# Performance work log

Hardware: AMD Instinct MI355X
Metric: run time of the kernel (lower is better)

## Reference

```python
import jax, jax.numpy as jnp
import numpy as np

NUM_HEADS = 16
HEAD_DIM = 64


def setup_inputs() -> dict:
    key = jax.random.key(0)
    ks = jax.random.split(key, 6)
    B, S, E = 4, 1024, 1024
    return {
        "x": jax.random.normal(ks[0], (B, S, E), dtype=jnp.float32),
        "W_qkv": jax.random.normal(ks[1], (E, 3 * E), dtype=jnp.float32) * 0.02,
        "b_qkv": jax.random.normal(ks[2], (3 * E,), dtype=jnp.float32) * 0.02,
        "pe": jax.random.normal(ks[3], (S, S, HEAD_DIM), dtype=jnp.float32) * 0.02,
        "W_out": jax.random.normal(ks[4], (E, E), dtype=jnp.float32) * 0.02,
        "b_out": jax.random.normal(ks[5], (E,), dtype=jnp.float32) * 0.02,
    }


def reference(x, W_qkv, b_qkv, pe, W_out, b_out):
    B, S, E = x.shape
    H, D = NUM_HEADS, HEAD_DIM
    scale = D ** -0.5
    # qkv projection: (B,S,3E) -> (3,B,H,S,D)
    qkv = (x @ W_qkv + b_qkv).reshape(B, S, 3, H, D).transpose(2, 0, 3, 1, 4)
    q, k, v = qkv[0], qkv[1], qkv[2]
    # raw scaled scores (NO softmax in original module)
    scores = jnp.einsum('bhxd,bhyd->bhxy', q, k) * scale
    # relative position bias: pe is (S,S,D) == (x,y,c); original permutes to (c,x,y)
    # then einsum('cxy,bnxc->bnxy', pe, q) -> equivalent to 'xyc,bhxc->bhxy'
    pe_q = jnp.einsum('xyc,bhxc->bhxy', pe, q) * scale
    attn = (scores + pe_q) @ v                      # (B,H,S,D)
    out = attn.transpose(0, 2, 1, 3).reshape(B, S, E)
    return out @ W_out + b_out
```

## Files before the change

### kernel.cpp

```cpp
#include <hip/hip_runtime.h>
#include <cstdint>
#include <cstddef>


typedef unsigned short u16;
typedef unsigned char  u8;
typedef __bf16 bf16x8 __attribute__((ext_vector_type(8)));
typedef float  f32x4  __attribute__((ext_vector_type(4)));
typedef unsigned short u16x8 __attribute__((ext_vector_type(8)));

#define MFMA16(a, b, c) __builtin_amdgcn_mfma_f32_16x16x32_bf16((a), (b), (c), 0, 0, 0)

#define GLOAD16(g, l)                                                        \
    __builtin_amdgcn_global_load_lds(                                        \
        (const __attribute__((address_space(1))) unsigned int*)(g),          \
        (__attribute__((address_space(3))) unsigned int*)(l), 16, 0, 0)

__device__ __forceinline__ u16 f2bf(float f) {
    __bf16 h = (__bf16)f;
    return __builtin_bit_cast(u16, h);
}
__device__ __forceinline__ u16x8 pack8(float4 a, float4 b) {
    u16x8 v;
    v[0] = f2bf(a.x); v[1] = f2bf(a.y); v[2] = f2bf(a.z); v[3] = f2bf(a.w);
    v[4] = f2bf(b.x); v[5] = f2bf(b.y); v[6] = f2bf(b.z); v[7] = f2bf(b.w);
    return v;
}

__device__ __forceinline__ void convT_tile(const float* __restrict__ in,
                                           u16* __restrict__ out, int R, int C,
                                           int bx, int by, float (*tile)[68]) {
    const int t  = threadIdx.x;
    const int r0 = by * 64, c0 = bx * 64;
    const int rr = t >> 4, c4 = t & 15;
    for (int p = 0; p < 4; ++p) {
        int r = rr + p * 16;
        float4 v = *(const float4*)&in[(size_t)(r0 + r) * C + c0 + c4 * 4];
        *(float4*)&tile[r][c4 * 4] = v;
    }
    __syncthreads();
    for (int p = 0; p < 4; ++p) {
        int n = rr + p * 16;
        ushort4 o;
        o.x = f2bf(tile[c4 * 4 + 0][n]);
        o.y = f2bf(tile[c4 * 4 + 1][n]);
        o.z = f2bf(tile[c4 * 4 + 2][n]);
        o.w = f2bf(tile[c4 * 4 + 3][n]);
        *(ushort4*)&out[(size_t)(c0 + n) * R + r0 + c4 * 4] = o;
    }
}

__global__ __launch_bounds__(256) void kprep(const float* __restrict__ x,
                                             u16* __restrict__ xb,
                                             const float* __restrict__ Wqkv,
                                             u16* __restrict__ wqkvT,
                                             const float* __restrict__ Wout,
                                             u16* __restrict__ woutT) {
    __shared__ float tile[64][68];
    const int bid = blockIdx.x;
    if (bid < 2048) {
        int i = (bid * 256 + threadIdx.x) * 8;
        float4 f0 = *(const float4*)&x[i];
        float4 f1 = *(const float4*)&x[i + 4];
        *(u16x8*)&xb[i] = pack8(f0, f1);
    } else if (bid < 2816) {
        int r = bid - 2048;
        convT_tile(Wqkv, wqkvT, 1024, 3072, r % 48, r / 48, tile);
    } else {
        int r = bid - 2816;
        convT_tile(Wout, woutT, 1024, 1024, r % 16, r / 16, tile);
    }
}

__global__ __launch_bounds__(256, 2) void kgemm_qkv(const u16* __restrict__ A,
                                                    const u16* __restrict__ WT,
                                                    const float* __restrict__ bias,
                                                    u16* __restrict__ qb,
                                                    u16* __restrict__ kb,
                                                    u16* __restrict__ vtb) {
    __shared__ u16 a_s[128 * 64];
    __shared__ u16 b_s[128 * 64];
    const int t = threadIdx.x;
    const int m0 = blockIdx.y * 128, n0 = blockIdx.x * 128;
    const int lane = t & 63, w = t >> 6, lm = lane & 15, lq = lane >> 4;
    const int mb = (w >> 1) * 64, nb = (w & 1) * 64;
    const int sr = t >> 3, sc = (t & 7) * 8;

    f32x4 acc[4][4] = {};
    for (int k0 = 0; k0 < 1024; k0 += 64) {
        __syncthreads();
#pragma unroll
        for (int p = 0; p < 4; ++p) {
            GLOAD16(&A [(size_t)(m0 + p * 32 + sr) * 1024 + k0 + sc], &a_s[p * 2048 + t * 8]);
            GLOAD16(&WT[(size_t)(n0 + p * 32 + sr) * 1024 + k0 + sc], &b_s[p * 2048 + t * 8]);
        }
        __syncthreads();
#pragma unroll
        for (int ks = 0; ks < 2; ++ks) {
            bf16x8 af[4], bfr[4];
#pragma unroll
            for (int mt = 0; mt < 4; ++mt)
                af[mt] = *(const bf16x8*)&a_s[(mb + mt * 16 + lm) * 64 + ks * 32 + lq * 8];
#pragma unroll
            for (int nt = 0; nt < 4; ++nt)
                bfr[nt] = *(const bf16x8*)&b_s[(nb + nt * 16 + lm) * 64 + ks * 32 + lq * 8];
#pragma unroll
            for (int mt = 0; mt < 4; ++mt)
#pragma unroll
                for (int nt = 0; nt < 4; ++nt)
                    acc[mt][nt] = MFMA16(af[mt], bfr[nt], acc[mt][nt]);
        }
    }
    for (int nt = 0; nt < 4; ++nt) {
        int col = n0 + nb + nt * 16 + lm;
        float bv = bias[col];
        int which = col >> 10;
        int h = (col >> 6) & 15, d = col & 63;
        for (int mt = 0; mt < 4; ++mt) {
            int row0 = m0 + mb + mt * 16 + lq * 4;
            int b = row0 >> 10, s = row0 & 1023;
            if (which == 2) {
                ushort4 o;
                o.x = f2bf(acc[mt][nt][0] + bv);
                o.y = f2bf(acc[mt][nt][1] + bv);
                o.z = f2bf(acc[mt][nt][2] + bv);
                o.w = f2bf(acc[mt][nt][3] + bv);
                *(ushort4*)&vtb[((size_t)(b * 16 + h) * 64 + d) * 1024 + s] = o;
            } else {
                u16* dst = (which == 0) ? qb : kb;
                for (int i = 0; i < 4; ++i)
                    dst[((size_t)((b * 16 + h) * 1024 + s + i)) * 64 + d] =
                        f2bf(acc[mt][nt][i] + bv);
            }
        }
    }
}

__global__ __launch_bounds__(256, 4) void kpq(const u16* __restrict__ qb,
                                              const float* __restrict__ pe,
                                              u8* __restrict__ Pq) {
    __shared__ u16 q_s[64 * 64];
    __shared__ u16 pe_s[2][64 * 80];
    const int x = blockIdx.x;
    const int t = threadIdx.x;
    const int lane = t & 63, w = t >> 6, lm = lane & 15, lq = lane >> 4;
#pragma unroll
    for (int p = 0; p < 2; ++p)
        GLOAD16(&qb[(size_t)((p * 32 + (t >> 3)) * 1024 + x) * 64 + (t & 7) * 8],
                &q_s[p * 2048 + t * 8]);
    const int yl = t >> 2, cq = (t & 3) * 16;
    const float* pex = pe + (size_t)x * 65536;
    float4 r0, r1, r2, r3;
    {
        const float* src = &pex[(size_t)yl * 64 + cq];
        r0 = *(const float4*)&src[0];  r1 = *(const float4*)&src[4];
        r2 = *(const float4*)&src[8];  r3 = *(const float4*)&src[12];
    }
    u8* pq_base = Pq + ((size_t)lm * 1024 + x) * 1024 + lq * 16 + w * 4;
    int cur = 0;
    for (int it = 0; it < 16; ++it) {
        *(u16x8*)&pe_s[cur][yl * 80 + cq]     = pack8(r0, r1);
        *(u16x8*)&pe_s[cur][yl * 80 + cq + 8] = pack8(r2, r3);
        __syncthreads();
        if (it < 15) {
            const float* src = &pex[(size_t)((it + 1) * 64 + yl) * 64 + cq];
            r0 = *(const float4*)&src[0];  r1 = *(const float4*)&src[4];
            r2 = *(const float4*)&src[8];  r3 = *(const float4*)&src[12];
        }
        f32x4 acc[4] = {};
#pragma unroll
        for (int ks = 0; ks < 2; ++ks) {
            bf16x8 a = *(const bf16x8*)&pe_s[cur][(16 * w + lm) * 80 + ks * 32 + lq * 8];
#pragma unroll
            for (int nt = 0; nt < 4; ++nt) {
                bf16x8 b = *(const bf16x8*)&q_s[(nt * 16 + lm) * 64 + ks * 32 + lq * 8];
                acc[nt] = MFMA16(a, b, acc[nt]);
            }
        }
#pragma unroll
        for (int nt = 0; nt < 4; ++nt) {
            unsigned int pw;
            pw = __builtin_amdgcn_cvt_pk_fp8_f32(acc[nt][0], acc[nt][1], 0u, false);
            pw = __builtin_amdgcn_cvt_pk_fp8_f32(acc[nt][2], acc[nt][3], pw, true);
            *(unsigned int*)&pq_base[(size_t)nt * 16 * 1024 * 1024 + it * 64] = pw;
        }
        cur ^= 1;
    }
}

__global__ __launch_bounds__(256, 2) void kattn(const u16* __restrict__ qb,
                                                const u16* __restrict__ kb,
                                                const u16* __restrict__ vt,
                                                const u8* __restrict__ Pq,
                                                u16* __restrict__ attnb) {
    __shared__ u16 q_s[128 * 64];
    __shared__ u16 k_s[64 * 64];
    __shared__ u16 v_s[64 * 64];
    __shared__ u16 s_s[128 * 80];
    const int bid = blockIdx.x;
    const int bh = bid & 63, x0 = (bid >> 6) * 128;
    const int t = threadIdx.x;
    const int lane = t & 63, w = t >> 6, lm = lane & 15, lq = lane >> 4;
    const int sr = t >> 3, sc = (t & 7) * 8;

#pragma unroll
    for (int p = 0; p < 4; ++p)
        GLOAD16(&qb[(size_t)(bh * 1024 + x0 + p * 32 + sr) * 64 + sc],
                &q_s[p * 2048 + t * 8]);

    const u8* PqRow = Pq + ((size_t)(bh * 1024) + x0 + 32 * w + lm) * 1024 + lq * 16;
    f32x4 oacc[2][4] = {};
    for (int y0 = 0; y0 < 1024; y0 += 64) {
        uint4 pq4[2];
#pragma unroll
        for (int nt = 0; nt < 2; ++nt)
            pq4[nt] = *(const uint4*)&PqRow[(size_t)(nt * 16) * 1024 + y0];
        __syncthreads();
#pragma unroll
        for (int p = 0; p < 2; ++p) {
            GLOAD16(&kb[(size_t)(bh * 1024 + y0 + p * 32 + sr) * 64 + sc],
                    &k_s[p * 2048 + t * 8]);
            GLOAD16(&vt[(size_t)(bh * 64 + p * 32 + sr) * 1024 + y0 + sc],
                    &v_s[p * 2048 + t * 8]);
        }
        __syncthreads();
        f32x4 sacc[4][2] = {};
#pragma unroll
        for (int ks = 0; ks < 2; ++ks) {
            bf16x8 bq[2];
#pragma unroll
            for (int nt = 0; nt < 2; ++nt)
                bq[nt] = *(const bf16x8*)&q_s[(32 * w + nt * 16 + lm) * 64 + ks * 32 + lq * 8];
#pragma unroll
            for (int mt = 0; mt < 4; ++mt) {
                bf16x8 ak = *(const bf16x8*)&k_s[(mt * 16 + lm) * 64 + ks * 32 + lq * 8];
#pragma unroll
                for (int nt = 0; nt < 2; ++nt)
                    sacc[mt][nt] = MFMA16(ak, bq[nt], sacc[mt][nt]);
            }
        }
#pragma unroll
        for (int nt = 0; nt < 2; ++nt) {
            int xl = 32 * w + nt * 16 + lm;
            const unsigned int* pqc = (const unsigned int*)&pq4[nt];
#pragma unroll
            for (int mt = 0; mt < 4; ++mt) {
                unsigned int pw = pqc[mt];
                ushort4 o;
                o.x = f2bf((sacc[mt][nt][0] + __builtin_amdgcn_cvt_f32_fp8(pw, 0)) * 0.125f);
                o.y = f2bf((sacc[mt][nt][1] + __builtin_amdgcn_cvt_f32_fp8(pw, 1)) * 0.125f);
                o.z = f2bf((sacc[mt][nt][2] + __builtin_amdgcn_cvt_f32_fp8(pw, 2)) * 0.125f);
                o.w = f2bf((sacc[mt][nt][3] + __builtin_amdgcn_cvt_f32_fp8(pw, 3)) * 0.125f);
                *(ushort4*)&s_s[xl * 80 + mt * 16 + lq * 4] = o;
            }
        }
#pragma unroll
        for (int ks = 0; ks < 2; ++ks) {
            bf16x8 as[2];
#pragma unroll
            for (int mt = 0; mt < 2; ++mt)
                as[mt] = *(const bf16x8*)&s_s[(32 * w + mt * 16 + lm) * 80 + ks * 32 + lq * 8];
#pragma unroll
            for (int nt = 0; nt < 4; ++nt) {
                bf16x8 bv = *(const bf16x8*)&v_s[(nt * 16 + lm) * 64 + ks * 32 + lq * 8];
#pragma unroll
                for (int mt = 0; mt < 2; ++mt)
                    oacc[mt][nt] = MFMA16(as[mt], bv, oacc[mt][nt]);
            }
        }
    }
    const int b = bh >> 4, h = bh & 15;
    for (int mt = 0; mt < 2; ++mt) {
        for (int nt = 0; nt < 4; ++nt) {
            int d = nt * 16 + lm;
            for (int i = 0; i < 4; ++i) {
                int s = x0 + 32 * w + mt * 16 + lq * 4 + i;
                attnb[((size_t)(b * 1024 + s)) * 1024 + h * 64 + d] = f2bf(oacc[mt][nt][i]);
            }
        }
    }
}

__global__ __launch_bounds__(256, 2) void kgemm_out(const u16* __restrict__ A,
                                                    const u16* __restrict__ WT,
                                                    const float* __restrict__ bias,
                                                    float* __restrict__ out) {
    __shared__ u16 a_s[128 * 64];
    __shared__ u16 b_s[128 * 64];
    const int t = threadIdx.x;
    const int m0 = blockIdx.y * 128, n0 = blockIdx.x * 128;
    const int lane = t & 63, w = t >> 6, lm = lane & 15, lq = lane >> 4;
    const int mb = (w >> 1) * 64, nb = (w & 1) * 64;
    const int sr = t >> 3, sc = (t & 7) * 8;

    f32x4 acc[4][4] = {};
    for (int k0 = 0; k0 < 1024; k0 += 64) {
        __syncthreads();
#pragma unroll
        for (int p = 0; p < 4; ++p) {
            GLOAD16(&A [(size_t)(m0 + p * 32 + sr) * 1024 + k0 + sc], &a_s[p * 2048 + t * 8]);
            GLOAD16(&WT[(size_t)(n0 + p * 32 + sr) * 1024 + k0 + sc], &b_s[p * 2048 + t * 8]);
        }
        __syncthreads();
#pragma unroll
        for (int ks = 0; ks < 2; ++ks) {
            bf16x8 af[4], bfr[4];
#pragma unroll
            for (int mt = 0; mt < 4; ++mt)
                af[mt] = *(const bf16x8*)&a_s[(mb + mt * 16 + lm) * 64 + ks * 32 + lq * 8];
#pragma unroll
            for (int nt = 0; nt < 4; ++nt)
                bfr[nt] = *(const bf16x8*)&b_s[(nb + nt * 16 + lm) * 64 + ks * 32 + lq * 8];
#pragma unroll
            for (int mt = 0; mt < 4; ++mt)
#pragma unroll
                for (int nt = 0; nt < 4; ++nt)
                    acc[mt][nt] = MFMA16(af[mt], bfr[nt], acc[mt][nt]);
        }
    }
    for (int nt = 0; nt < 4; ++nt) {
        int col = n0 + nb + nt * 16 + lm;
        float bv = bias[col];
        for (int mt = 0; mt < 4; ++mt) {
            for (int i = 0; i < 4; ++i) {
                int row = m0 + mb + mt * 16 + lq * 4 + i;
                out[(size_t)row * 1024 + col] = acc[mt][nt][i] + bv;
            }
        }
    }
}

extern "C" void kernel_launch(void* const* d_in, const int* in_sizes, int n_in,
                              void* d_out, int out_size, void* d_ws, size_t ws_size,
                              hipStream_t stream) {
    (void)in_sizes; (void)n_in; (void)out_size; (void)ws_size;
    const float* x    = (const float*)d_in[0];
    const float* Wqkv = (const float*)d_in[1];
    const float* bqkv = (const float*)d_in[2];
    const float* pe   = (const float*)d_in[3];
    const float* Wout = (const float*)d_in[4];
    const float* bout = (const float*)d_in[5];
    float* out = (float*)d_out;

    char* ws = (char*)d_ws;
    u16* xb    = (u16*)ws;  ws += (size_t)4096 * 1024 * 2;
    u16* wqkvT = (u16*)ws;  ws += (size_t)3072 * 1024 * 2;
    u16* woutT = (u16*)ws;  ws += (size_t)1024 * 1024 * 2;
    u16* qb    = (u16*)ws;  ws += (size_t)64 * 1024 * 64 * 2;
    u16* kb    = (u16*)ws;  ws += (size_t)64 * 1024 * 64 * 2;
    u16* vtb   = (u16*)ws;  ws += (size_t)64 * 64 * 1024 * 2;
    u16* attnb = (u16*)ws;  ws += (size_t)4 * 1024 * 1024 * 2;
    u8*  pq    = (u8*)ws;   ws += (size_t)64 * 1024 * 1024;

    kprep<<<3072, 256, 0, stream>>>(x, xb, Wqkv, wqkvT, Wout, woutT);
    kgemm_qkv<<<dim3(24, 32), 256, 0, stream>>>(xb, wqkvT, bqkv, qb, kb, vtb);
    kpq<<<1024, 256, 0, stream>>>(qb, pe, pq);
    kattn<<<512, 256, 0, stream>>>(qb, kb, vtb, pq, attnb);
    kgemm_out<<<dim3(8, 32), 256, 0, stream>>>(attnb, woutT, bout, out);
}
```

Baseline: 521.8 us.

## Rewrite QKV GEMM with 256x256 tiles and 4-stage async LDS pipeline

Restructures the QKV projection GEMM to use 512-thread blocks computing 256x256 output tiles, with a four-deep ring of LDS buffers filled by direct global-to-LDS loads issued several k-steps ahead. Raw s_barrier plus explicit vmcnt waits and s_setprio around MFMA bursts replace the per-iteration __syncthreads load/compute serialization. The aim is to hide global load latency and raise arithmetic intensity per block. The cost is only 192 blocks, which may underfill the GPU, along with higher register pressure from 32 accumulators per wave.

```diff
diff --git a/kernel.cpp b/kernel.cpp
--- a/kernel.cpp
+++ b/kernel.cpp
@@ -25,6 +25,16 @@
     v[0] = f2bf(a.x); v[1] = f2bf(a.y); v[2] = f2bf(a.z); v[3] = f2bf(a.w);
     v[4] = f2bf(b.x); v[5] = f2bf(b.y); v[6] = f2bf(b.z); v[7] = f2bf(b.w);
     return v;
+}
+
+__device__ __forceinline__ void sbar() {
+    asm volatile("" ::: "memory");
+    __builtin_amdgcn_s_barrier();
+    asm volatile("" ::: "memory");
+}
+template <int N> __device__ __forceinline__ void waitv() {
+    if constexpr (N >= 0)
+        asm volatile("s_waitcnt vmcnt(%0)" :: "n"(N) : "memory");
 }
 
 __device__ __forceinline__ void convT_tile(const float* __restrict__ in,
@@ -72,65 +82,104 @@
     }
 }
 
-__global__ __launch_bounds__(256, 2) void kgemm_qkv(const u16* __restrict__ A,
+#define STAGE_A(kt) {                                                         \
+    u16* d_ = &a_s[(kt) & 3][t * 8];                                          \
+    const u16* g_ = &A[(size_t)(m0g + (t >> 2)) * 1024 + (kt) * 32 + (t & 3) * 8]; \
+    GLOAD16(g_, d_);                                                          \
+    GLOAD16(g_ + (size_t)128 * 1024, d_ + 4096); }
+
+#define STAGE_B(kt) {                                                         \
+    u16* d_ = &b_s[(kt) & 3][t * 8];                                          \
+    const u16* g_ = &WT[(size_t)(n0g + (t >> 2)) * 1024 + (kt) * 32 + (t & 3) * 8]; \
+    GLOAD16(g_, d_);                                                          \
+    GLOAD16(g_ + (size_t)128 * 1024, d_ + 4096); }
+
+#define QKV_GROUP(g, DOSTAGE, GATEN)                                          \
+  {                                                                           \
+    const int s_ = (g) & 3;                                                   \
+                                       \
+    _Pragma("unroll")                                                         \
+    for (int mf = 0; mf < 4; ++mf)                                            \
+      af[mf] = *(const bf16x8*)&a_s[s_][(wr * 128 + mf * 16 + lm) * 32 + lq * 8]; \
+    _Pragma("unroll")                                                         \
+    for (int nf = 0; nf < 4; ++nf)                                            \
+      bfr[nf] = *(const bf16x8*)&b_s[s_][(wc * 64 + nf * 16 + lm) * 32 + lq * 8]; \
+    if (DOSTAGE) STAGE_A((g) + 3);                                            \
+    sbar();                                                                   \
+    __builtin_amdgcn_s_setprio(1);                                            \
+    _Pragma("unroll")                                                         \
+    for (int mf = 0; mf < 4; ++mf)                                            \
+      _Pragma("unroll")                                                       \
+      for (int nf = 0; nf < 4; ++nf)                                          \
+        acc[mf][nf] = MFMA16(af[mf], bfr[nf], acc[mf][nf]);                   \
+    __builtin_amdgcn_s_setprio(0);                                            \
+    sbar();                                                                   \
+                  \
+    _Pragma("unroll")                                                         \
+    for (int mf = 0; mf < 4; ++mf)                                            \
+      af[mf] = *(const bf16x8*)&a_s[s_][(wr * 128 + 64 + mf * 16 + lm) * 32 + lq * 8]; \
+    if (DOSTAGE) STAGE_B((g) + 3);                                            \
+    waitv<GATEN>();                                                           \
+    sbar();                                                                   \
+    __builtin_amdgcn_s_setprio(1);                                            \
+    _Pragma("unroll")                                                         \
+    for (int mf = 0; mf < 4; ++mf)                                            \
+      _Pragma("unroll")                                                       \
+      for (int nf = 0; nf < 4; ++nf)                                          \
+        acc[4 + mf][nf] = MFMA16(af[mf], bfr[nf], acc[4 + mf][nf]);           \
+    __builtin_amdgcn_s_setprio(0);                                            \
+    sbar();                                                                   \
+  }
+
+__global__ __launch_bounds__(512, 2) void kgemm_qkv(const u16* __restrict__ A,
                                                     const u16* __restrict__ WT,
                                                     const float* __restrict__ bias,
                                                     u16* __restrict__ qb,
                                                     u16* __restrict__ kb,
                                                     u16* __restrict__ vtb) {
-    __shared__ u16 a_s[128 * 64];
-    __shared__ u16 b_s[128 * 64];
+    __shared__ u16 a_s[4][256 * 32];
+    __shared__ u16 b_s[4][256 * 32];
     const int t = threadIdx.x;
-    const int m0 = blockIdx.y * 128, n0 = blockIdx.x * 128;
+    const int m0g = blockIdx.y * 256, n0g = blockIdx.x * 256;
     const int lane = t & 63, w = t >> 6, lm = lane & 15, lq = lane >> 4;
-    const int mb = (w >> 1) * 64, nb = (w & 1) * 64;
-    const int sr = t >> 3, sc = (t & 7) * 8;
-
-    f32x4 acc[4][4] = {};
-    for (int k0 = 0; k0 < 1024; k0 += 64) {
-        __syncthreads();
-#pragma unroll
-        for (int p = 0; p < 4; ++p) {
-            GLOAD16(&A [(size_t)(m0 + p * 32 + sr) * 1024 + k0 + sc], &a_s[p * 2048 + t * 8]);
-            GLOAD16(&WT[(size_t)(n0 + p * 32 + sr) * 1024 + k0 + sc], &b_s[p * 2048 + t * 8]);
-        }
-        __syncthreads();
-#pragma unroll
-        for (int ks = 0; ks < 2; ++ks) {
-            bf16x8 af[4], bfr[4];
-#pragma unroll
-            for (int mt = 0; mt < 4; ++mt)
-                af[mt] = *(const bf16x8*)&a_s[(mb + mt * 16 + lm) * 64 + ks * 32 + lq * 8];
-#pragma unroll
-            for (int nt = 0; nt < 4; ++nt)
-                bfr[nt] = *(const bf16x8*)&b_s[(nb + nt * 16 + lm) * 64 + ks * 32 + lq * 8];
-#pragma unroll
-            for (int mt = 0; mt < 4; ++mt)
-#pragma unroll
-                for (int nt = 0; nt < 4; ++nt)
-                    acc[mt][nt] = MFMA16(af[mt], bfr[nt], acc[mt][nt]);
-        }
-    }
-    for (int nt = 0; nt < 4; ++nt) {
-        int col = n0 + nb + nt * 16 + lm;
+    const int wr = w >> 2, wc = w & 3;
+
+    f32x4 acc[8][4] = {};
+    bf16x8 af[4], bfr[4];
+
+    STAGE_A(0); STAGE_B(0);
+    STAGE_A(1); STAGE_B(1);
+    STAGE_A(2); STAGE_B(2);
+    waitv<8>();
+    sbar();
+
+#pragma unroll 1
+    for (int g = 0; g < 29; ++g)
+        QKV_GROUP(g, true, 8);
+    QKV_GROUP(29, false, 4);
+    QKV_GROUP(30, false, 0);
+    QKV_GROUP(31, false, -1);
+
+    for (int nf = 0; nf < 4; ++nf) {
+        int col = n0g + wc * 64 + nf * 16 + lm;
         float bv = bias[col];
         int which = col >> 10;
         int h = (col >> 6) & 15, d = col & 63;
-        for (int mt = 0; mt < 4; ++mt) {
-            int row0 = m0 + mb + mt * 16 + lq * 4;
+        for (int mf = 0; mf < 8; ++mf) {
+            int row0 = m0g + wr * 128 + mf * 16 + lq * 4;
             int b = row0 >> 10, s = row0 & 1023;
             if (which == 2) {
                 ushort4 o;
-                o.x = f2bf(acc[mt][nt][0] + bv);
-                o.y = f2bf(acc[mt][nt][1] + bv);
-                o.z = f2bf(acc[mt][nt][2] + bv);
-                o.w = f2bf(acc[mt][nt][3] + bv);
+                o.x = f2bf(acc[mf][nf][0] + bv);
+                o.y = f2bf(acc[mf][nf][1] + bv);
+                o.z = f2bf(acc[mf][nf][2] + bv);
+                o.w = f2bf(acc[mf][nf][3] + bv);
                 *(ushort4*)&vtb[((size_t)(b * 16 + h) * 64 + d) * 1024 + s] = o;
             } else {
                 u16* dst = (which == 0) ? qb : kb;
                 for (int i = 0; i < 4; ++i)
                     dst[((size_t)((b * 16 + h) * 1024 + s + i)) * 64 + d] =
-                        f2bf(acc[mt][nt][i] + bv);
+                        f2bf(acc[mf][nf][i] + bv);
             }
         }
     }
@@ -353,7 +402,7 @@
     u8*  pq    = (u8*)ws;   ws += (size_t)64 * 1024 * 1024;
 
     kprep<<<3072, 256, 0, stream>>>(x, xb, Wqkv, wqkvT, Wout, woutT);
-    kgemm_qkv<<<dim3(24, 32), 256, 0, stream>>>(xb, wqkvT, bqkv, qb, kb, vtb);
+    kgemm_qkv<<<dim3(12, 16), 512, 0, stream>>>(xb, wqkvT, bqkv, qb, kb, vtb);
     kpq<<<1024, 256, 0, stream>>>(qb, pe, pq);
     kattn<<<512, 256, 0, stream>>>(qb, kb, vtb, pq, attnb);
     kgemm_out<<<dim3(8, 32), 256, 0, stream>>>(attnb, woutT, bout, out);
```

After: 527.8 us. No clear change (+1.1%).

## Double-buffer K/V tiles in attention kernel with async prefetch

Applied to the files above, without the earlier changes.

Splits the attention kernel's K and V shared-memory tiles into two buffers. The loads for the next 64-key tile are issued before computing on the current one, and explicit vmcnt waits plus raw barriers replace the two __syncthreads per iteration. This is meant to hide global-to-LDS load latency behind the MFMA work. In exchange it raises LDS use to about 68KB per block, which may limit occupancy, and relies on hand-counted outstanding-load numbers being correct.

```diff
diff --git a/kernel.cpp b/kernel.cpp
--- a/kernel.cpp
+++ b/kernel.cpp
@@ -25,6 +25,15 @@
     v[0] = f2bf(a.x); v[1] = f2bf(a.y); v[2] = f2bf(a.z); v[3] = f2bf(a.w);
     v[4] = f2bf(b.x); v[5] = f2bf(b.y); v[6] = f2bf(b.z); v[7] = f2bf(b.w);
     return v;
+}
+
+__device__ __forceinline__ void sbar() {
+    asm volatile("" ::: "memory");
+    __builtin_amdgcn_s_barrier();
+    asm volatile("" ::: "memory");
+}
+template <int N> __device__ __forceinline__ void waitv() {
+    asm volatile("s_waitcnt vmcnt(%0)" :: "n"(N) : "memory");
 }
 
 __device__ __forceinline__ void convT_tile(const float* __restrict__ in,
@@ -194,8 +203,8 @@
                                                 const u8* __restrict__ Pq,
                                                 u16* __restrict__ attnb) {
     __shared__ u16 q_s[128 * 64];
-    __shared__ u16 k_s[64 * 64];
-    __shared__ u16 v_s[64 * 64];
+    __shared__ u16 k_s[2][64 * 64];
+    __shared__ u16 v_s[2][64 * 64];
     __shared__ u16 s_s[128 * 80];
     const int bid = blockIdx.x;
     const int bh = bid & 63, x0 = (bid >> 6) * 128;
@@ -207,68 +216,100 @@
     for (int p = 0; p < 4; ++p)
         GLOAD16(&qb[(size_t)(bh * 1024 + x0 + p * 32 + sr) * 64 + sc],
                 &q_s[p * 2048 + t * 8]);
+#pragma unroll
+    for (int p = 0; p < 2; ++p) {
+        GLOAD16(&kb[(size_t)(bh * 1024 + p * 32 + sr) * 64 + sc],
+                &k_s[0][p * 2048 + t * 8]);
+        GLOAD16(&vt[(size_t)(bh * 64 + p * 32 + sr) * 1024 + sc],
+                &v_s[0][p * 2048 + t * 8]);
+    }
 
     const u8* PqRow = Pq + ((size_t)(bh * 1024) + x0 + 32 * w + lm) * 1024 + lq * 16;
     f32x4 oacc[2][4] = {};
-    for (int y0 = 0; y0 < 1024; y0 += 64) {
+
+#define ATTN_COMPUTE(CUR, Y0)                                                  \
+    {                                                                          \
+                 \
+        f32x4 sacc[4][2] = {};                                                 \
+        _Pragma("unroll")                                                      \
+        for (int ks = 0; ks < 2; ++ks) {                                       \
+            bf16x8 bq[2];                                                      \
+            _Pragma("unroll")                                                  \
+            for (int nt = 0; nt < 2; ++nt)                                     \
+                bq[nt] = *(const bf16x8*)&q_s[(32 * w + nt * 16 + lm) * 64 + ks * 32 + lq * 8]; \
+            _Pragma("unroll")                                                  \
+            for (int mt = 0; mt < 4; ++mt) {                                   \
+                bf16x8 ak = *(const bf16x8*)&k_s[CUR][(mt * 16 + lm) * 64 + ks * 32 + lq * 8]; \
+                _Pragma("unroll")                                              \
+                for (int nt = 0; nt < 2; ++nt)                                 \
+                    sacc[mt][nt] = MFMA16(ak, bq[nt], sacc[mt][nt]);           \
+            }                                                                  \
+        }                                                                      \
+                \
+        _Pragma("unroll")                                                      \
+        for (int nt = 0; nt < 2; ++nt) {                                       \
+            int xl = 32 * w + nt * 16 + lm;                                    \
+            const unsigned int* pqc = (const unsigned int*)&pq4[nt];           \
+            _Pragma("unroll")                                                  \
+            for (int mt = 0; mt < 4; ++mt) {                                   \
+                unsigned int pw = pqc[mt];                                     \
+                ushort4 o;                                                     \
+                o.x = f2bf((sacc[mt][nt][0] + __builtin_amdgcn_cvt_f32_fp8(pw, 0)) * 0.125f); \
+                o.y = f2bf((sacc[mt][nt][1] + __builtin_amdgcn_cvt_f32_fp8(pw, 1)) * 0.125f); \
+                o.z = f2bf((sacc[mt][nt][2] + __builtin_amdgcn_cvt_f32_fp8(pw, 2)) * 0.125f); \
+                o.w = f2bf((sacc[mt][nt][3] + __builtin_amdgcn_cvt_f32_fp8(pw, 3)) * 0.125f); \
+                *(ushort4*)&s_s[xl * 80 + mt * 16 + lq * 4] = o;               \
+            }                                                                  \
+        }                                                                      \
+                                   \
+        _Pragma("unroll")                                                      \
+        for (int ks = 0; ks < 2; ++ks) {                                       \
+            bf16x8 as[2];                                                      \
+            _Pragma("unroll")                                                  \
+            for (int mt = 0; mt < 2; ++mt)                                     \
+                as[mt] = *(const bf16x8*)&s_s[(32 * w + mt * 16 + lm) * 80 + ks * 32 + lq * 8]; \
+            _Pragma("unroll")                                                  \
+            for (int nt = 0; nt < 4; ++nt) {                                   \
+                bf16x8 bv = *(const bf16x8*)&v_s[CUR][(nt * 16 + lm) * 64 + ks * 32 + lq * 8]; \
+                _Pragma("unroll")                                              \
+                for (int mt = 0; mt < 2; ++mt)                                 \
+                    oacc[mt][nt] = MFMA16(as[mt], bv, oacc[mt][nt]);           \
+            }                                                                  \
+        }                                                                      \
+    }
+
+    int cur = 0;
+#pragma unroll 1
+    for (int it = 0; it < 15; ++it) {
+        const int y0 = it * 64;
+        sbar();
+#pragma unroll
+        for (int p = 0; p < 2; ++p) {
+            GLOAD16(&kb[(size_t)(bh * 1024 + y0 + 64 + p * 32 + sr) * 64 + sc],
+                    &k_s[cur ^ 1][p * 2048 + t * 8]);
+            GLOAD16(&vt[(size_t)(bh * 64 + p * 32 + sr) * 1024 + y0 + 64 + sc],
+                    &v_s[cur ^ 1][p * 2048 + t * 8]);
+        }
         uint4 pq4[2];
 #pragma unroll
         for (int nt = 0; nt < 2; ++nt)
             pq4[nt] = *(const uint4*)&PqRow[(size_t)(nt * 16) * 1024 + y0];
-        __syncthreads();
-#pragma unroll
-        for (int p = 0; p < 2; ++p) {
-            GLOAD16(&kb[(size_t)(bh * 1024 + y0 + p * 32 + sr) * 64 + sc],
-                    &k_s[p * 2048 + t * 8]);
-            GLOAD16(&vt[(size_t)(bh * 64 + p * 32 + sr) * 1024 + y0 + sc],
-                    &v_s[p * 2048 + t * 8]);
-        }
-        __syncthreads();
-        f32x4 sacc[4][2] = {};
-#pragma unroll
-        for (int ks = 0; ks < 2; ++ks) {
-            bf16x8 bq[2];
-#pragma unroll
-            for (int nt = 0; nt < 2; ++nt)
-                bq[nt] = *(const bf16x8*)&q_s[(32 * w + nt * 16 + lm) * 64 + ks * 32 + lq * 8];
-#pragma unroll
-            for (int mt = 0; mt < 4; ++mt) {
-                bf16x8 ak = *(const bf16x8*)&k_s[(mt * 16 + lm) * 64 + ks * 32 + lq * 8];
-#pragma unroll
-                for (int nt = 0; nt < 2; ++nt)
-                    sacc[mt][nt] = MFMA16(ak, bq[nt], sacc[mt][nt]);
-            }
-        }
-#pragma unroll
-        for (int nt = 0; nt < 2; ++nt) {
-            int xl = 32 * w + nt * 16 + lm;
-            const unsigned int* pqc = (const unsigned int*)&pq4[nt];
-#pragma unroll
-            for (int mt = 0; mt < 4; ++mt) {
-                unsigned int pw = pqc[mt];
-                ushort4 o;
-                o.x = f2bf((sacc[mt][nt][0] + __builtin_amdgcn_cvt_f32_fp8(pw, 0)) * 0.125f);
-                o.y = f2bf((sacc[mt][nt][1] + __builtin_amdgcn_cvt_f32_fp8(pw, 1)) * 0.125f);
-                o.z = f2bf((sacc[mt][nt][2] + __builtin_amdgcn_cvt_f32_fp8(pw, 2)) * 0.125f);
-                o.w = f2bf((sacc[mt][nt][3] + __builtin_amdgcn_cvt_f32_fp8(pw, 3)) * 0.125f);
-                *(ushort4*)&s_s[xl * 80 + mt * 16 + lq * 4] = o;
-            }
-        }
-#pragma unroll
-        for (int ks = 0; ks < 2; ++ks) {
-            bf16x8 as[2];
-#pragma unroll
-            for (int mt = 0; mt < 2; ++mt)
-                as[mt] = *(const bf16x8*)&s_s[(32 * w + mt * 16 + lm) * 80 + ks * 32 + lq * 8];
-#pragma unroll
-            for (int nt = 0; nt < 4; ++nt) {
-                bf16x8 bv = *(const bf16x8*)&v_s[(nt * 16 + lm) * 64 + ks * 32 + lq * 8];
-#pragma unroll
-                for (int mt = 0; mt < 2; ++mt)
-                    oacc[mt][nt] = MFMA16(as[mt], bv, oacc[mt][nt]);
-            }
-        }
-    }
+        waitv<6>();
+        sbar();
+        ATTN_COMPUTE(cur, y0)
+        cur ^= 1;
+    }
+    {
+        uint4 pq4[2];
+#pragma unroll
+        for (int nt = 0; nt < 2; ++nt)
+            pq4[nt] = *(const uint4*)&PqRow[(size_t)(nt * 16) * 1024 + 960];
+        waitv<2>();
+        sbar();
+        ATTN_COMPUTE(cur, 960)
+    }
+#undef ATTN_COMPUTE
+
     const int b = bh >> 4, h = bh & 15;
     for (int mt = 0; mt < 2; ++mt) {
         for (int nt = 0; nt < 4; ++nt) {
```

After: 519.9 us (median of 2 runs). No clear change (-0.4%).
